# Optimization experiments

Measured on AMD Instinct MI355X. Metric: run time of the kernel, lower is better.

## Reference

```python
import jax, jax.numpy as jnp
import numpy as np

B = 512      # batch
L = 20       # reviews per user/item (L1 == L2)
N = 100      # words per review (must match between user/item, required by original bmm)
V = 50000    # vocab
D = 64       # word_dim
E = 32       # id_emb_size
U = 20000    # user_num
I = 20000    # item_num
H = 3        # point_num_heads
NT, NM = 10, 12  # travel type / month cardinalities


def _lin(x, W, b):
    # torch nn.Linear: x @ W.T + b, W is [out, in]
    return x @ W.T + b


def _hard_gumbel(logits, g):
    # F.gumbel_softmax(hard=True, tau=1, dim=1); g is pre-sampled standard Gumbel noise
    y = jax.nn.softmax(logits + g, axis=1)
    hard = jax.nn.one_hot(jnp.argmax(y, axis=1), logits.shape[1], dtype=y.dtype)
    return hard - jax.lax.stop_gradient(y) + y  # straight-through


def _coatt(u_fea, i_fea, M, Wu, bu, Wi, bi, pooling, gumbel_noise=None):
    # u_fea: [B, L1, d]; i_fea: [B, L2, d]
    u = _lin(u_fea, Wu, bu)
    i = _lin(i_fea, Wi, bi)
    S = jnp.einsum('bld,de,bme->blm', u, M, i)  # [B, L1, L2]
    if pooling == 'max':
        u_score, i_score = S.max(axis=2), S.max(axis=1)
    else:
        u_score, i_score = S.mean(axis=2), S.mean(axis=1)
    if gumbel_noise is not None:
        gu, gi = gumbel_noise
        p_u, p_i = _hard_gumbel(u_score, gu), _hard_gumbel(i_score, gi)
    else:
        p_u, p_i = jax.nn.softmax(u_score, axis=1), jax.nn.softmax(i_score, axis=1)
    return p_u[..., None], p_i[..., None]  # [B, L1, 1], [B, L2, 1]


def setup_inputs() -> dict:
    key = jax.random.key(0)
    ks = iter(jax.random.split(key, 48))
    unif = lambda shape, s=0.1: jax.random.uniform(next(ks), shape, minval=-s, maxval=s, dtype=jnp.float32)
    xav = lambda shape: jax.random.normal(next(ks), shape, dtype=jnp.float32) * np.sqrt(2.0 / (shape[-1] + shape[-2]))
    inp = {}
    inp['user_reviews'] = jax.random.randint(next(ks), (B, L, N), 0, V)
    inp['item_reviews'] = jax.random.randint(next(ks), (B, L, N), 0, V)
    inp['uids'] = jax.random.randint(next(ks), (B,), 0, U)
    inp['iids'] = jax.random.randint(next(ks), (B,), 0, I)
    inp['travel_type'] = jax.random.randint(next(ks), (B,), 0, NT)
    inp['travel_month'] = jax.random.randint(next(ks), (B,), 0, NM)
    # pre-sampled standard Gumbel noise for the hard pointer selection (one per head)
    inp['gnoise_u'] = -jnp.log(-jnp.log(jax.random.uniform(next(ks), (H, B, L), minval=1e-20, maxval=1.0)))
    inp['gnoise_i'] = -jnp.log(-jnp.log(jax.random.uniform(next(ks), (H, B, L), minval=1e-20, maxval=1.0)))
    # embedding tables
    inp['user_word_embs'] = unif((V, D))
    inp['item_word_embs'] = unif((V, D))
    inp['user_id_table'] = unif((U, E), 1.0)
    inp['item_id_table'] = unif((I, E), 1.0)
    inp['type_table'] = unif((NT, E), 1.0)
    inp['month_table'] = unif((NM, E), 1.0)
    # review gate
    inp['fc_g1_w'] = unif((D, D)); inp['fc_g1_b'] = unif((D,))
    inp['fc_g2_w'] = unif((D, D)); inp['fc_g2_b'] = unif((D,))
    # per-head co-attention params (stacked over H)
    inp['M_r'] = xav((H, D, D)); inp['Wu_r'] = unif((H, D, D)); inp['bu_r'] = unif((H, D))
    inp['Wi_r'] = unif((H, D, D)); inp['bi_r'] = unif((H, D))
    inp['M_w'] = xav((H, D, D)); inp['Wu_w'] = unif((H, D, D)); inp['bu_w'] = unif((H, D))
    inp['Wi_w'] = unif((H, D, D)); inp['bi_w'] = unif((H, D))
    inp['M_f'] = xav((H, E, E)); inp['Wu_f'] = unif((H, E, E)); inp['bu_f'] = unif((H, E))
    inp['Wi_f'] = unif((H, E, E)); inp['bi_f'] = unif((H, E))
    # projection layers
    inp['ufc_w'] = unif((E, D)); inp['ufc_b'] = unif((E,))
    inp['ifc_w'] = unif((E, D)); inp['ifc_b'] = unif((E,))
    inp['u_fc_w'] = unif((E, E * H)); inp['u_fc_b'] = unif((E,))
    inp['i_fc_w'] = unif((E, E * H)); inp['i_fc_b'] = unif((E,))
    return inp


def reference(user_reviews, item_reviews, uids, iids, travel_type, travel_month,
              gnoise_u, gnoise_i, user_word_embs, item_word_embs,
              user_id_table, item_id_table, type_table, month_table,
              fc_g1_w, fc_g1_b, fc_g2_w, fc_g2_b,
              M_r, Wu_r, bu_r, Wi_r, bi_r,
              M_w, Wu_w, bu_w, Wi_w, bi_w,
              M_f, Wu_f, bu_f, Wi_f, bi_f,
              ufc_w, ufc_b, ifc_w, ifc_b, u_fc_w, u_fc_b, i_fc_w, i_fc_b):
    # id-type embeddings -> feature stack [B, 4, E]
    user_id_emb = user_id_table[uids]
    item_id_emb = item_id_table[iids]
    type_emb = type_table[travel_type]
    month_emb = month_table[travel_month]
    feature_embedding = jnp.stack([user_id_emb, item_id_emb, type_emb, month_emb], axis=1)

    def review_gate(reviews_idx, table):
        s = table[reviews_idx].sum(axis=2)  # [B, L, N, D] -> [B, L, D]
        return jax.nn.sigmoid(_lin(s, fc_g1_w, fc_g1_b)) * jnp.tanh(_lin(s, fc_g2_w, fc_g2_b))

    u_reviews_g = review_gate(user_reviews, user_word_embs)
    i_reviews_g = review_gate(item_reviews, item_word_embs)

    u_feas, i_feas = [], []
    for h in range(H):
        # review-level pointer co-attention (hard gumbel, max pooling)
        p_u, p_i = _coatt(u_reviews_g, i_reviews_g, M_r[h], Wu_r[h], bu_r[h], Wi_r[h], bi_r[h],
                          pooling='max', gumbel_noise=(gnoise_u[h], gnoise_i[h]))
        # soft index -> cast to int (kills gradient, like torch .long()) -> word gather
        u_idx = jnp.einsum('bln,bl->bn', user_reviews.astype(p_u.dtype), p_u[..., 0]).astype(jnp.int32)
        i_idx = jnp.einsum('bln,bl->bn', item_reviews.astype(p_i.dtype), p_i[..., 0]).astype(jnp.int32)
        u_words = user_word_embs[u_idx]  # [B, N, D]
        i_words = item_word_embs[i_idx]
        # word-level co-attention (softmax, avg pooling)
        p_u2, p_i2 = _coatt(u_words, i_words, M_w[h], Wu_w[h], bu_w[h], Wi_w[h], bi_w[h], pooling='avg')
        u_w_fea = jnp.einsum('bnd,bn->bd', u_words, p_u2[..., 0])
        i_w_fea = jnp.einsum('bnd,bn->bd', u_words, p_i2[..., 0])  # NOTE: original uses u_words here (kept)
        ure = jax.nn.relu(_lin(u_w_fea, ufc_w, ufc_b))  # dropout = identity (eval)
        ire = jax.nn.relu(_lin(i_w_fea, ifc_w, ifc_b))
        review_embedding = jnp.stack([ure, ire], axis=1)  # [B, 2, E]
        review_att, fea_att = _coatt(review_embedding, feature_embedding,
                                     M_f[h], Wu_f[h], bu_f[h], Wi_f[h], bi_f[h], pooling='avg')
        fea_att_e = feature_embedding * fea_att  # [B, 4, E]
        user_id_e, item_id_e, type_e, month_e = (fea_att_e[:, 0], fea_att_e[:, 1],
                                                 fea_att_e[:, 2], fea_att_e[:, 3])
        rae = review_embedding * review_att
        user_fea_h = rae[:, 0]
        u_feas.append(user_fea_h)
        i_feas.append(user_fea_h)  # NOTE: original assigns item_fea from the user slice (kept)
    u_out = _lin(jnp.concatenate(u_feas, axis=1), u_fc_w, u_fc_b)
    i_out = _lin(jnp.concatenate(i_feas, axis=1), i_fc_w, i_fc_b)
    user_fea = jnp.stack([user_id_e, type_e, u_out], axis=1)   # [B, 3, E]
    item_fea = jnp.stack([item_id_e, month_e, i_out], axis=1)  # [B, 3, E]
    return user_fea, item_fea
```

## Files before the change

kernel.cpp:

```cpp
#include <hip/hip_runtime.h>
#include <math.h>

#define Bn 512
#define Ln 20
#define Nn 100
#define Dn 64
#define En 32
#define Hn 3

__global__ __launch_bounds__(256) void k0a_prep(
    const float* __restrict__ M_r, const float* __restrict__ Wu_r, const float* __restrict__ bu_r,
    const float* __restrict__ Wi_r,
    const float* __restrict__ M_w, const float* __restrict__ Wu_w, const float* __restrict__ bu_w,
    const float* __restrict__ Wi_w, const float* __restrict__ bi_w,
    const float* __restrict__ Wu_f, const float* __restrict__ Wi_f,
    const float* __restrict__ ufc, const float* __restrict__ ifc,
    const float* __restrict__ ufc2, const float* __restrict__ ifc2,
    float* __restrict__ WiT_r, float* __restrict__ WMr, float* __restrict__ bMr,
    float* __restrict__ P, float* __restrict__ Q, float* __restrict__ MB, float* __restrict__ MTB,
    float* __restrict__ WuT_f, float* __restrict__ WiT_f,
    float* __restrict__ ufcT, float* __restrict__ ifcT,
    float* __restrict__ u_fcT, float* __restrict__ i_fcT)
{
    int t = blockIdx.x * blockDim.x + threadIdx.x;
    int stride = gridDim.x * blockDim.x;
    for (int k = t; k < Hn*Dn*Dn; k += stride) {
        int h = k >> 12, r = k & 4095; int c = r >> 6, e = r & 63;
        const float* Wu = Wu_r + h*4096; const float* M = M_r + h*4096;
        float a = 0.f;
        for (int d = 0; d < Dn; ++d) a += Wu[d*Dn + c] * M[d*Dn + e];
        WMr[k] = a;
    }
    for (int k = t; k < Hn*Dn*Dn; k += stride) {
        int h = k >> 12, r = k & 4095; int d = r >> 6, bb = r & 63;
        const float* M = M_w + h*4096; const float* Wi = Wi_w + h*4096;
        float a = 0.f;
        for (int e = 0; e < Dn; ++e) a += M[d*Dn + e] * Wi[e*Dn + bb];
        P[k] = a;
    }
    for (int k = t; k < Hn*Dn*Dn; k += stride) {
        int h = k >> 12, r = k & 4095; int d = r >> 6, bb = r & 63;
        const float* M = M_w + h*4096; const float* Wu = Wu_w + h*4096;
        float a = 0.f;
        for (int e = 0; e < Dn; ++e) a += M[e*Dn + d] * Wu[e*Dn + bb];
        Q[k] = a;
    }
    for (int k = t; k < Hn*Dn*Dn; k += stride) {
        int h = k >> 12, r = k & 4095; int c = r >> 6, dp = r & 63;
        WiT_r[k] = Wi_r[h*4096 + dp*Dn + c];
    }
    for (int k = t; k < Hn*Dn; k += stride) {
        int h = k >> 6, e = k & 63;
        const float* M = M_r + h*4096;
        float a = 0.f;
        for (int d = 0; d < Dn; ++d) a += bu_r[h*Dn + d] * M[d*Dn + e];
        bMr[k] = a;
        const float* Mw_ = M_w + h*4096;
        float p = 0.f, q = 0.f;
        for (int d2 = 0; d2 < Dn; ++d2) {
            p += Mw_[e*Dn + d2] * bi_w[h*Dn + d2];
            q += Mw_[d2*Dn + e] * bu_w[h*Dn + d2];
        }
        MB[k] = p; MTB[k] = q;
    }
    for (int k = t; k < Hn*En*En; k += stride) {
        int h = k / (En*En); int rem = k - h*En*En;
        int a = rem >> 5, c = rem & 31;
        int src = h*En*En + c*En + a;
        WuT_f[k] = Wu_f[src]; WiT_f[k] = Wi_f[src];
    }
    for (int k = t; k < Dn*En; k += stride) {
        int d = k >> 5, e = k & 31;
        ufcT[k] = ufc[e*Dn + d]; ifcT[k] = ifc[e*Dn + d];
    }
    for (int k = t; k < 96*En; k += stride) {
        int kk = k >> 5, e = k & 31;
        u_fcT[k] = ufc2[e*96 + kk]; i_fcT[k] = ifc2[e*96 + kk];
    }
}

__global__ __launch_bounds__(256) void k0b_prep(
    const float* __restrict__ Wu_w, const float* __restrict__ Wi_w,
    const float* __restrict__ P, const float* __restrict__ Q,
    const float* __restrict__ MB, const float* __restrict__ MTB,
    float* __restrict__ GuT, float* __restrict__ GiT,
    float* __restrict__ gu_v, float* __restrict__ gi_v)
{
    int t = blockIdx.x * blockDim.x + threadIdx.x;
    int stride = gridDim.x * blockDim.x;
    for (int k = t; k < Hn*Dn*Dn; k += stride) {
        int h = k >> 12, r = k & 4095; int bb = r >> 6, a = r & 63;
        const float* Wu = Wu_w + h*4096; const float* Pp = P + h*4096;
        float s = 0.f;
        for (int d = 0; d < Dn; ++d) s += Wu[d*Dn + a] * Pp[d*Dn + bb];
        GuT[k] = s;
    }
    for (int k = t; k < Hn*Dn*Dn; k += stride) {
        int h = k >> 12, r = k & 4095; int bb = r >> 6, a = r & 63;
        const float* Wi = Wi_w + h*4096; const float* Qp = Q + h*4096;
        float s = 0.f;
        for (int d = 0; d < Dn; ++d) s += Wi[d*Dn + a] * Qp[d*Dn + bb];
        GiT[k] = s;
    }
    for (int k = t; k < Hn*Dn; k += stride) {
        int h = k >> 6, a = k & 63;
        const float* Wu = Wu_w + h*4096; const float* Wi = Wi_w + h*4096;
        float s1 = 0.f, s2 = 0.f;
        for (int d = 0; d < Dn; ++d) {
            s1 += Wu[d*Dn + a] * MB[h*Dn + d];
            s2 += Wi[d*Dn + a] * MTB[h*Dn + d];
        }
        gu_v[k] = s1; gi_v[k] = s2;
    }
}

__global__ __launch_bounds__(256) void k1a_gsum(
    const int* __restrict__ urev, const int* __restrict__ irev,
    const float* __restrict__ utab, const float* __restrict__ itab,
    float* __restrict__ sout)
{
    int tid = threadIdx.x;
    int ln = tid & 63;
    int wv = tid >> 6;
    int gw = blockIdx.x * 4 + wv;
    int side = (gw >= Bn*Ln);
    int r = gw - (side ? Bn*Ln : 0);
    const int* rev = side ? irev : urev;
    const float* tab = side ? itab : utab;
    int i0 = rev[r*Nn + ln];
    int i1 = (ln < Nn - 64) ? rev[r*Nn + 64 + ln] : 0;
    int r0 = ln >> 4;
    int q4 = (ln & 15) << 2;
    float4 buf[25];
    #pragma unroll
    for (int j = 0; j < 25; ++j) {
        int n = r0 + 4*j;
        int idx = (n < 64) ? __shfl(i0, n) : __shfl(i1, n - 64);
        buf[j] = *(const float4*)(tab + idx*Dn + q4);
    }
    float4 a = buf[0];
    #pragma unroll
    for (int j = 1; j < 25; ++j) { a.x += buf[j].x; a.y += buf[j].y; a.z += buf[j].z; a.w += buf[j].w; }
    a.x += __shfl_xor(a.x, 16); a.y += __shfl_xor(a.y, 16); a.z += __shfl_xor(a.z, 16); a.w += __shfl_xor(a.w, 16);
    a.x += __shfl_xor(a.x, 32); a.y += __shfl_xor(a.y, 32); a.z += __shfl_xor(a.z, 32); a.w += __shfl_xor(a.w, 32);
    if (ln < 16) *(float4*)(sout + gw*Dn + q4) = a;
}

__global__ __launch_bounds__(256) void k1b_gate(
    const float* __restrict__ sin,
    const float* __restrict__ W1, const float* __restrict__ b1v,
    const float* __restrict__ W2, const float* __restrict__ b2v,
    float* __restrict__ ugo, float* __restrict__ igo)
{
    __shared__ float w1s[Dn][Dn+1];
    __shared__ float w2s[Dn][Dn+1];
    int tid = threadIdx.x;
    for (int k = tid; k < Dn*Dn; k += 256) {
        int r = k >> 6, c = k & 63;
        w1s[r][c] = W1[k]; w2s[r][c] = W2[k];
    }
    __syncthreads();
    int ln = tid & 63;
    int wv = tid >> 6;
    float b1 = b1v[ln], b2 = b2v[ln];
    int nW = gridDim.x * 4;
    for (int gw = blockIdx.x * 4 + wv; gw < 2*Bn*Ln; gw += nW) {
        float sv = sin[gw*Dn + ln];
        float t1 = b1, t2 = b2;
        #pragma unroll 8
        for (int d = 0; d < Dn; ++d) {
            float sd = __shfl(sv, d);
            t1 += sd * w1s[ln][d];
            t2 += sd * w2s[ln][d];
        }
        float g = (1.f / (1.f + expf(-t1))) * tanhf(t2);
        int side = (gw >= Bn*Ln);
        int r = gw - (side ? Bn*Ln : 0);
        (side ? igo : ugo)[r*Dn + ln] = g;
    }
}

__global__ __launch_bounds__(256, 4) void k2_coatt(
    const int* __restrict__ urev, const int* __restrict__ irev,
    const int* __restrict__ uids, const int* __restrict__ iids,
    const int* __restrict__ ttype, const int* __restrict__ tmonth,
    const float* __restrict__ gu_all, const float* __restrict__ gi_all,
    const float* __restrict__ utab, const float* __restrict__ itab,
    const float* __restrict__ uid_tab, const float* __restrict__ iid_tab,
    const float* __restrict__ type_tab, const float* __restrict__ month_tab,
    const float* __restrict__ ug_in, const float* __restrict__ ig_in,
    const float* __restrict__ WMr, const float* __restrict__ bMr,
    const float* __restrict__ WiT_r, const float* __restrict__ bi_r,
    const float* __restrict__ GuT, const float* __restrict__ GiT,
    const float* __restrict__ gu_v, const float* __restrict__ gi_v,
    const float* __restrict__ M_f, const float* __restrict__ bu_f, const float* __restrict__ bi_f,
    const float* __restrict__ WuT_f, const float* __restrict__ WiT_f,
    const float* __restrict__ ufcT, const float* __restrict__ ufc_bv,
    const float* __restrict__ ifcT, const float* __restrict__ ifc_bv,
    float* __restrict__ feas, float* __restrict__ outp)
{
    __shared__ __align__(16) float pool[6400];
    __shared__ float vecs[4][Dn];
    __shared__ float sc[2][Nn];
    __shared__ float uif[2][Dn];
    __shared__ float att[6];
    __shared__ int   lstar[2];

    int tid = threadIdx.x;
    int bh = blockIdx.x;
    int b = bh / Hn;
    int h = bh - b*Hn;
    int ln = tid & 63;
    int wv = tid >> 6;

    {
        const float4* su = (const float4*)(ug_in + b*Ln*Dn);
        const float4* si = (const float4*)(ig_in + b*Ln*Dn);
        float4* du = (float4*)pool;
        float4* di = (float4*)(pool + 1280);
        for (int k = tid; k < (Ln*Dn)/4; k += 256) { du[k] = su[k]; di[k] = si[k]; }
    }
    __syncthreads();

    {
        int iside = wv >> 1;
        int lbase = (wv & 1) * 10;
        const float* W = (iside ? (WiT_r + h*4096) : (WMr + h*4096)) + ln;
        const float* X = pool + (iside ? 1280 : 0);
        float bias = iside ? bi_r[h*Dn + ln] : bMr[h*Dn + ln];
        float acc[10];
        #pragma unroll
        for (int l = 0; l < 10; ++l) acc[l] = 0.f;
        for (int dd = 0; dd < Dn; dd += 4) {
            float w0 = W[(dd+0)*Dn];
            float w1 = W[(dd+1)*Dn];
            float w2 = W[(dd+2)*Dn];
            float w3 = W[(dd+3)*Dn];
            #pragma unroll
            for (int l = 0; l < 10; ++l) {
                float4 x = *(const float4*)(X + (lbase+l)*Dn + dd);
                acc[l] += x.x*w0 + x.y*w1 + x.z*w2 + x.w*w3;
            }
        }
        float* out = pool + (iside ? 3840 : 2560);
        #pragma unroll
        for (int l = 0; l < 10; ++l) {
            int lg = lbase + l;
            out[lg*Dn + (ln ^ lg)] = acc[l] + bias;
        }
    }
    __syncthreads();
    for (int k = tid; k < Ln*Ln; k += 256) {
        int l = k / Ln, m = k - l*Ln;
        const float* Ab = pool + 2560 + l*Dn;
        const float* iv = pool + 3840 + m*Dn;
        float a = 0.f;
        for (int e = 0; e < Dn; ++e) a += Ab[e ^ l] * iv[e ^ m];
        pool[5120 + k] = a;
    }
    __syncthreads();
    if (wv == 0) {
        float v = -3.4e38f;
        if (ln < Ln) {
            float mx = pool[5120 + ln*Ln];
            #pragma unroll
            for (int m = 1; m < Ln; ++m) mx = fmaxf(mx, pool[5120 + ln*Ln + m]);
            v = mx + gu_all[(h*Bn + b)*Ln + ln];
        }
        int idx = ln;
        #pragma unroll
        for (int off = 32; off > 0; off >>= 1) {
            float ov = __shfl_down(v, off);
            int oi = __shfl_down(idx, off);
            if (ov > v || (ov == v && oi < idx)) { v = ov; idx = oi; }
        }
        if (ln == 0) lstar[0] = idx;
    } else if (wv == 1) {
        float v = -3.4e38f;
        if (ln < Ln) {
            float mx = pool[5120 + ln];
            #pragma unroll
            for (int l = 1; l < Ln; ++l) mx = fmaxf(mx, pool[5120 + l*Ln + ln]);
            v = mx + gi_all[(h*Bn + b)*Ln + ln];
        }
        int idx = ln;
        #pragma unroll
        for (int off = 32; off > 0; off >>= 1) {
            float ov = __shfl_down(v, off);
            int oi = __shfl_down(idx, off);
            if (ov > v || (ov == v && oi < idx)) { v = ov; idx = oi; }
        }
        if (ln == 0) lstar[1] = idx;
    }
    __syncthreads();

    int rubase = (b*Ln + lstar[0])*Nn;
    int ribase = (b*Ln + lstar[1])*Nn;
    int r0 = ln >> 4;
    int q4 = (ln & 15) << 2;
    int idxr[25];

    if (wv < 2) {
        for (int k = tid; k < Nn*16; k += 128) {
            int n = k >> 4, qi = k & 15;
            int idx = urev[rubase + n];
            float4 v = *(const float4*)(utab + idx*Dn + (qi << 2));
            *(float4*)(pool + n*Dn + (((qi ^ (n & 15)) << 2))) = v;
        }
    } else {
        const int* rev = (wv == 2) ? irev : urev;
        const float* tab = (wv == 2) ? itab : utab;
        int rb = (wv == 2) ? ribase : rubase;
        #pragma unroll
        for (int j = 0; j < 25; ++j) idxr[j] = rev[rb + r0 + 4*j];
        float4 s = make_float4(0.f, 0.f, 0.f, 0.f);
        #pragma unroll 5
        for (int g = 0; g < 5; ++g) {
            float4 v0 = *(const float4*)(tab + idxr[g*5+0]*Dn + q4);
            float4 v1 = *(const float4*)(tab + idxr[g*5+1]*Dn + q4);
            float4 v2 = *(const float4*)(tab + idxr[g*5+2]*Dn + q4);
            float4 v3 = *(const float4*)(tab + idxr[g*5+3]*Dn + q4);
            float4 v4 = *(const float4*)(tab + idxr[g*5+4]*Dn + q4);
            s.x += v0.x+v1.x+v2.x+v3.x+v4.x;
            s.y += v0.y+v1.y+v2.y+v3.y+v4.y;
            s.z += v0.z+v1.z+v2.z+v3.z+v4.z;
            s.w += v0.w+v1.w+v2.w+v3.w+v4.w;
        }
        s.x += __shfl_xor(s.x, 16); s.y += __shfl_xor(s.y, 16); s.z += __shfl_xor(s.z, 16); s.w += __shfl_xor(s.w, 16);
        s.x += __shfl_xor(s.x, 32); s.y += __shfl_xor(s.y, 32); s.z += __shfl_xor(s.z, 32); s.w += __shfl_xor(s.w, 32);
        if (ln < 16) {
            float4 m = make_float4(s.x*(1.f/Nn), s.y*(1.f/Nn), s.z*(1.f/Nn), s.w*(1.f/Nn));
            *(float4*)(&vecs[(wv == 2) ? 1 : 0][q4]) = m;
        }
    }
    __syncthreads();

    if (tid < Dn) {
        float a = gu_v[h*Dn + tid];
        for (int bb = 0; bb < Dn; ++bb) a += GuT[h*4096 + bb*Dn + tid] * vecs[1][bb];
        vecs[2][tid] = a;
    } else if (tid < 2*Dn) {
        int aa = tid - Dn;
        float a = gi_v[h*Dn + aa];
        for (int bb = 0; bb < Dn; ++bb) a += GiT[h*4096 + bb*Dn + aa] * vecs[0][bb];
        vecs[3][aa] = a;
    }
    __syncthreads();

    if (tid < Nn) {
        float a = 0.f;
        const float* row = pool + tid*Dn;
        int sw = tid & 15;
        #pragma unroll
        for (int qi = 0; qi < 16; ++qi) {
            float4 w = *(const float4*)(&vecs[2][qi << 2]);
            float4 x = *(const float4*)(row + ((qi ^ sw) << 2));
            a += x.x*w.x + x.y*w.y + x.z*w.z + x.w*w.w;
        }
        sc[0][tid] = a;
    } else if (wv == 2) {
        float4 wq = *(const float4*)(&vecs[3][q4]);
        #pragma unroll 5
        for (int g = 0; g < 5; ++g) {
            float p0, p1, p2, p3, p4;
            {
                float4 v0 = *(const float4*)(itab + idxr[g*5+0]*Dn + q4);
                float4 v1 = *(const float4*)(itab + idxr[g*5+1]*Dn + q4);
                float4 v2 = *(const float4*)(itab + idxr[g*5+2]*Dn + q4);
                float4 v3 = *(const float4*)(itab + idxr[g*5+3]*Dn + q4);
                float4 v4 = *(const float4*)(itab + idxr[g*5+4]*Dn + q4);
                p0 = v0.x*wq.x + v0.y*wq.y + v0.z*wq.z + v0.w*wq.w;
                p1 = v1.x*wq.x + v1.y*wq.y + v1.z*wq.z + v1.w*wq.w;
                p2 = v2.x*wq.x + v2.y*wq.y + v2.z*wq.z + v2.w*wq.w;
                p3 = v3.x*wq.x + v3.y*wq.y + v3.z*wq.z + v3.w*wq.w;
                p4 = v4.x*wq.x + v4.y*wq.y + v4.z*wq.z + v4.w*wq.w;
            }
            #pragma unroll
            for (int off = 1; off < 16; off <<= 1) {
                p0 += __shfl_xor(p0, off); p1 += __shfl_xor(p1, off);
                p2 += __shfl_xor(p2, off); p3 += __shfl_xor(p3, off);
                p4 += __shfl_xor(p4, off);
            }
            if ((ln & 15) == 0) {
                sc[1][r0 + 4*(g*5+0)] = p0;
                sc[1][r0 + 4*(g*5+1)] = p1;
                sc[1][r0 + 4*(g*5+2)] = p2;
                sc[1][r0 + 4*(g*5+3)] = p3;
                sc[1][r0 + 4*(g*5+4)] = p4;
            }
        }
    }
    __syncthreads();
    if (wv == 0 || wv == 2) {
        float* s = sc[wv >> 1];
        float x0 = s[ln];
        float x1 = (ln < Nn - 64) ? s[64 + ln] : -3.4e38f;
        float mx = fmaxf(x0, x1);
        #pragma unroll
        for (int off = 32; off > 0; off >>= 1) mx = fmaxf(mx, __shfl_xor(mx, off));
        float e0 = expf(x0 - mx);
        float e1 = (ln < Nn - 64) ? expf(x1 - mx) : 0.f;
        float sum = e0 + e1;
        #pragma unroll
        for (int off = 32; off > 0; off >>= 1) sum += __shfl_xor(sum, off);
        float inv = 1.f / sum;
        s[ln] = e0 * inv;
        if (ln < Nn - 64) s[64 + ln] = e1 * inv;
    }
    __syncthreads();
    if (tid < 2*Dn) {
        int which = tid >> 6;
        int d = tid & 63;
        int qt = (d >> 2), dl = d & 3;
        const float* p = sc[which];
        float a = 0.f;
        for (int n = 0; n < Nn; ++n)
            a += p[n] * pool[n*Dn + ((qt ^ (n & 15)) << 2) + dl];
        uif[which][d] = a;
    }
    __syncthreads();
    float* fe_ = pool;
    float* re_ = pool + 128;
    float* u3_ = pool + 192;
    float* i3_ = pool + 256;
    float* A3_ = pool + 384;
    if (tid < En) {
        float a = ufc_bv[tid];
        for (int d = 0; d < Dn; ++d) a += uif[0][d] * ufcT[d*En + tid];
        re_[tid] = fmaxf(a, 0.f);
    } else if (tid < 2*En) {
        int e = tid - En;
        float a = ifc_bv[e];
        for (int d = 0; d < Dn; ++d) a += uif[1][d] * ifcT[d*En + e];
        re_[En + e] = fmaxf(a, 0.f);
    } else if (tid < 2*En + 4*En) {
        int j = tid - 2*En;
        int rrow = j >> 5, e = j & 31;
        float v;
        if (rrow == 0) v = uid_tab[uids[b]*En + e];
        else if (rrow == 1) v = iid_tab[iids[b]*En + e];
        else if (rrow == 2) v = type_tab[ttype[b]*En + e];
        else v = month_tab[tmonth[b]*En + e];
        fe_[j] = v;
    }
    __syncthreads();
    const float* WuTf = WuT_f + h*En*En;
    const float* WiTf = WiT_f + h*En*En;
    const float* Mf   = M_f  + h*En*En;
    if (tid < 2*En) {
        int l = tid >> 5, e = tid & 31;
        float a = bu_f[h*En + e];
        for (int j = 0; j < En; ++j) a += re_[l*En + j] * WuTf[j*En + e];
        u3_[tid] = a;
    } else if (tid < 6*En) {
        int t2 = tid - 2*En;
        int m = t2 >> 5, e = t2 & 31;
        float a = bi_f[h*En + e];
        for (int j = 0; j < En; ++j) a += fe_[m*En + j] * WiTf[j*En + e];
        i3_[t2] = a;
    }
    __syncthreads();
    if (tid < 2*En) {
        int l = tid >> 5, e = tid & 31;
        float a = 0.f;
        for (int d = 0; d < En; ++d) a += u3_[l*En + d] * Mf[d*En + e];
        A3_[tid] = a;
    }
    __syncthreads();
    if (tid == 0) {
        float S3[2][4];
        for (int l = 0; l < 2; ++l)
            for (int m = 0; m < 4; ++m) {
                float a = 0.f;
                for (int e = 0; e < En; ++e) a += A3_[l*En + e] * i3_[m*En + e];
                S3[l][m] = a;
            }
        float us0 = (S3[0][0] + S3[0][1] + S3[0][2] + S3[0][3]) * 0.25f;
        float us1 = (S3[1][0] + S3[1][1] + S3[1][2] + S3[1][3]) * 0.25f;
        float mx = fmaxf(us0, us1);
        float e0 = expf(us0 - mx), e1 = expf(us1 - mx);
        float inv = 1.f / (e0 + e1);
        att[0] = e0 * inv; att[1] = e1 * inv;
        float is_[4]; float mxi = -3.4e38f;
        for (int m = 0; m < 4; ++m) { is_[m] = (S3[0][m] + S3[1][m]) * 0.5f; mxi = fmaxf(mxi, is_[m]); }
        float ssum = 0.f, ee[4];
        for (int m = 0; m < 4; ++m) { ee[m] = expf(is_[m] - mxi); ssum += ee[m]; }
        float invi = 1.f / ssum;
        for (int m = 0; m < 4; ++m) att[2 + m] = ee[m] * invi;
    }
    __syncthreads();
    if (tid < En) {
        feas[b*96 + h*En + tid] = re_[tid] * att[0];
    }
    if (h == 2) {
        if (tid >= 32 && tid < 64)        { int e = tid - 32;  outp[b*96 + e]              = fe_[e]      * att[2]; }
        else if (tid >= 64 && tid < 96)   { int e = tid - 64;  outp[b*96 + 32 + e]         = fe_[64 + e] * att[4]; }
        else if (tid >= 96 && tid < 128)  { int e = tid - 96;  outp[Bn*96 + b*96 + e]      = fe_[32 + e] * att[3]; }
        else if (tid >= 128 && tid < 160) { int e = tid - 128; outp[Bn*96 + b*96 + 32 + e] = fe_[96 + e] * att[5]; }
    }
}

__global__ __launch_bounds__(64) void k3_final(
    const float* __restrict__ feas,
    const float* __restrict__ u_fcT, const float* __restrict__ u_fc_bv,
    const float* __restrict__ i_fcT, const float* __restrict__ i_fc_bv,
    float* __restrict__ outp)
{
    __shared__ float f[96];
    int b = blockIdx.x, tid = threadIdx.x;
    for (int k = tid; k < 96; k += 64) f[k] = feas[b*96 + k];
    __syncthreads();
    if (tid < 32) {
        float a = u_fc_bv[tid];
        for (int k = 0; k < 96; ++k) a += f[k] * u_fcT[k*32 + tid];
        outp[b*96 + 64 + tid] = a;
    } else {
        int e = tid - 32;
        float a = i_fc_bv[e];
        for (int k = 0; k < 96; ++k) a += f[k] * i_fcT[k*32 + e];
        outp[Bn*96 + b*96 + 64 + e] = a;
    }
}

extern "C" void kernel_launch(void* const* d_in, const int* in_sizes, int n_in,
                              void* d_out, int out_size, void* d_ws, size_t ws_size,
                              hipStream_t stream)
{
    const int* urev = (const int*)d_in[0];
    const int* irev = (const int*)d_in[1];
    const int* uids = (const int*)d_in[2];
    const int* iids = (const int*)d_in[3];
    const int* ttype = (const int*)d_in[4];
    const int* tmonth = (const int*)d_in[5];
    const float* gu = (const float*)d_in[6];
    const float* gi = (const float*)d_in[7];
    const float* utab = (const float*)d_in[8];
    const float* itab = (const float*)d_in[9];
    const float* uid_tab = (const float*)d_in[10];
    const float* iid_tab = (const float*)d_in[11];
    const float* type_tab = (const float*)d_in[12];
    const float* month_tab = (const float*)d_in[13];
    const float* fc_g1_w = (const float*)d_in[14];
    const float* fc_g1_b = (const float*)d_in[15];
    const float* fc_g2_w = (const float*)d_in[16];
    const float* fc_g2_b = (const float*)d_in[17];
    const float* M_r = (const float*)d_in[18];
    const float* Wu_r = (const float*)d_in[19];
    const float* bu_r = (const float*)d_in[20];
    const float* Wi_r = (const float*)d_in[21];
    const float* bi_r = (const float*)d_in[22];
    const float* M_w = (const float*)d_in[23];
    const float* Wu_w = (const float*)d_in[24];
    const float* bu_w = (const float*)d_in[25];
    const float* Wi_w = (const float*)d_in[26];
    const float* bi_w = (const float*)d_in[27];
    const float* M_f = (const float*)d_in[28];
    const float* Wu_f = (const float*)d_in[29];
    const float* bu_f = (const float*)d_in[30];
    const float* Wi_f = (const float*)d_in[31];
    const float* bi_f = (const float*)d_in[32];
    const float* ufc_w = (const float*)d_in[33];
    const float* ufc_b = (const float*)d_in[34];
    const float* ifc_w = (const float*)d_in[35];
    const float* ifc_b = (const float*)d_in[36];
    const float* u_fc_w = (const float*)d_in[37];
    const float* u_fc_b = (const float*)d_in[38];
    const float* i_fc_w = (const float*)d_in[39];
    const float* i_fc_b = (const float*)d_in[40];
    (void)in_sizes; (void)n_in; (void)out_size; (void)ws_size;

    float* ws = (float*)d_ws;
    float* ugo   = ws;
    float* igo   = ugo + Bn*Ln*Dn;
    float* sgat  = igo + Bn*Ln*Dn;
    float* feas  = sgat + 2*Bn*Ln*Dn;
    float* WiT_r = feas + Bn*96;
    float* WMr   = WiT_r + Hn*Dn*Dn;
    float* bMr   = WMr + Hn*Dn*Dn;
    float* P     = bMr + Hn*Dn;
    float* Q     = P + Hn*Dn*Dn;
    float* MB    = Q + Hn*Dn*Dn;
    float* MTB   = MB + Hn*Dn;
    float* GuT   = MTB + Hn*Dn;
    float* GiT   = GuT + Hn*Dn*Dn;
    float* gu_v  = GiT + Hn*Dn*Dn;
    float* gi_v  = gu_v + Hn*Dn;
    float* WuT_f = gi_v + Hn*Dn;
    float* WiT_f = WuT_f + Hn*En*En;
    float* ufcT  = WiT_f + Hn*En*En;
    float* ifcT  = ufcT + Dn*En;
    float* u_fcT = ifcT + Dn*En;
    float* i_fcT = u_fcT + 96*En;

    hipLaunchKernelGGL(k0a_prep, dim3(48), dim3(256), 0, stream,
        M_r, Wu_r, bu_r, Wi_r, M_w, Wu_w, bu_w, Wi_w, bi_w,
        Wu_f, Wi_f, ufc_w, ifc_w, u_fc_w, i_fc_w,
        WiT_r, WMr, bMr, P, Q, MB, MTB, WuT_f, WiT_f, ufcT, ifcT, u_fcT, i_fcT);

    hipLaunchKernelGGL(k0b_prep, dim3(48), dim3(256), 0, stream,
        Wu_w, Wi_w, P, Q, MB, MTB, GuT, GiT, gu_v, gi_v);

    hipLaunchKernelGGL(k1a_gsum, dim3(2*Bn*Ln/4), dim3(256), 0, stream,
        urev, irev, utab, itab, sgat);

    hipLaunchKernelGGL(k1b_gate, dim3(512), dim3(256), 0, stream,
        sgat, fc_g1_w, fc_g1_b, fc_g2_w, fc_g2_b, ugo, igo);

    hipLaunchKernelGGL(k2_coatt, dim3(Bn*Hn), dim3(256), 0, stream,
        urev, irev, uids, iids, ttype, tmonth, gu, gi, utab, itab,
        uid_tab, iid_tab, type_tab, month_tab, ugo, igo,
        WMr, bMr, WiT_r, bi_r, GuT, GiT, gu_v, gi_v,
        M_f, bu_f, bi_f, WuT_f, WiT_f,
        ufcT, ufc_b, ifcT, ifc_b, feas, (float*)d_out);

    hipLaunchKernelGGL(k3_final, dim3(Bn), dim3(64), 0, stream,
        feas, u_fcT, u_fc_b, i_fcT, i_fc_b, (float*)d_out);
}
```

Baseline: 326.7 us.

## Fuse weight-folding prep kernels into one LDS-staged per-head kernel

Replaces the two grid-stride prep kernels (P/Q, then GuT/GiT) with a single kernel that stages each head's M, Wu and Wi matrices in shared memory and computes the intermediate products there, splitting outputs across 4 blocks per head. This removes the global round trip for P, Q, MB and MTB and one kernel launch. Each of the 4 blocks per head redundantly computes the full P/Q intermediates, and only 12 blocks run, so the work is less spread across the device. Transposes move into a separate small kernel.

New measurement: 347.5 us. +6.4%, slower.

```diff
diff --git a/kernel.cpp b/kernel.cpp
--- a/kernel.cpp
+++ b/kernel.cpp
@@ -8,16 +8,97 @@
 #define En 32
 #define Hn 3
 
-__global__ __launch_bounds__(256) void k0a_prep(
+__global__ __launch_bounds__(256) void k0_fold(
     const float* __restrict__ M_r, const float* __restrict__ Wu_r, const float* __restrict__ bu_r,
-    const float* __restrict__ Wi_r,
     const float* __restrict__ M_w, const float* __restrict__ Wu_w, const float* __restrict__ bu_w,
     const float* __restrict__ Wi_w, const float* __restrict__ bi_w,
+    float* __restrict__ WMr, float* __restrict__ bMr,
+    float* __restrict__ GuT, float* __restrict__ GiT,
+    float* __restrict__ gu_v, float* __restrict__ gi_v)
+{
+    __shared__ float A[4096], B2[4096], C2[4096], D2[4096], E2[4096];
+    __shared__ float MBs[64], MTBs[64];
+    int tid = threadIdx.x;
+    int h = blockIdx.x >> 2, sub = blockIdx.x & 3;
+    {
+        const float4* a = (const float4*)(M_w + h*4096);
+        const float4* bsrc = (const float4*)(Wu_w + h*4096);
+        const float4* c = (const float4*)(Wi_w + h*4096);
+        for (int k = tid; k < 1024; k += 256) {
+            ((float4*)A)[k] = a[k];
+            ((float4*)B2)[k] = bsrc[k];
+            ((float4*)C2)[k] = c[k];
+        }
+    }
+    __syncthreads();
+    for (int k = tid; k < 4096; k += 256) {
+        int d = k >> 6, b = k & 63;
+        float p = 0.f, q = 0.f;
+        for (int e = 0; e < 64; ++e) {
+            p += A[d*64 + e] * C2[e*64 + b];
+            q += A[e*64 + d] * B2[e*64 + b];
+        }
+        D2[k] = p; E2[k] = q;
+    }
+    if (sub == 0 && tid < 64) {
+        float p = 0.f, q = 0.f;
+        for (int e = 0; e < 64; ++e) {
+            p += A[tid*64 + e] * bi_w[h*64 + e];
+            q += A[e*64 + tid] * bu_w[h*64 + e];
+        }
+        MBs[tid] = p; MTBs[tid] = q;
+    }
+    __syncthreads();
+    #pragma unroll
+    for (int i = 0; i < 4; ++i) {
+        int k = sub*1024 + i*256 + tid;
+        int b = k >> 6, a = k & 63;
+        float s1 = 0.f, s2 = 0.f;
+        for (int d = 0; d < 64; ++d) {
+            s1 += B2[d*64 + a] * D2[d*64 + b];
+            s2 += C2[d*64 + a] * E2[d*64 + b];
+        }
+        GuT[h*4096 + k] = s1; GiT[h*4096 + k] = s2;
+    }
+    if (sub == 0 && tid < 64) {
+        float s1 = 0.f, s2 = 0.f;
+        for (int d = 0; d < 64; ++d) {
+            s1 += B2[d*64 + tid] * MBs[d];
+            s2 += C2[d*64 + tid] * MTBs[d];
+        }
+        gu_v[h*64 + tid] = s1; gi_v[h*64 + tid] = s2;
+    }
+    __syncthreads();
+    {
+        const float4* a = (const float4*)(M_r + h*4096);
+        const float4* bsrc = (const float4*)(Wu_r + h*4096);
+        for (int k = tid; k < 1024; k += 256) {
+            ((float4*)A)[k] = a[k];
+            ((float4*)B2)[k] = bsrc[k];
+        }
+    }
+    __syncthreads();
+    #pragma unroll
+    for (int i = 0; i < 4; ++i) {
+        int k = sub*1024 + i*256 + tid;
+        int c = k >> 6, e = k & 63;
+        float s = 0.f;
+        for (int d = 0; d < 64; ++d) s += B2[d*64 + c] * A[d*64 + e];
+        WMr[h*4096 + k] = s;
+    }
+    if (sub == 0 && tid < 64) {
+        float s = 0.f;
+        for (int d = 0; d < 64; ++d) s += bu_r[h*64 + d] * A[d*64 + tid];
+        bMr[h*64 + tid] = s;
+    }
+}
+
+__global__ __launch_bounds__(256) void k0_misc(
+    const float* __restrict__ Wi_r,
     const float* __restrict__ Wu_f, const float* __restrict__ Wi_f,
     const float* __restrict__ ufc, const float* __restrict__ ifc,
     const float* __restrict__ ufc2, const float* __restrict__ ifc2,
-    float* __restrict__ WiT_r, float* __restrict__ WMr, float* __restrict__ bMr,
-    float* __restrict__ P, float* __restrict__ Q, float* __restrict__ MB, float* __restrict__ MTB,
+    float* __restrict__ WiT_r,
     float* __restrict__ WuT_f, float* __restrict__ WiT_f,
     float* __restrict__ ufcT, float* __restrict__ ifcT,
     float* __restrict__ u_fcT, float* __restrict__ i_fcT)
@@ -25,43 +106,8 @@
     int t = blockIdx.x * blockDim.x + threadIdx.x;
     int stride = gridDim.x * blockDim.x;
     for (int k = t; k < Hn*Dn*Dn; k += stride) {
-        int h = k >> 12, r = k & 4095; int c = r >> 6, e = r & 63;
-        const float* Wu = Wu_r + h*4096; const float* M = M_r + h*4096;
-        float a = 0.f;
-        for (int d = 0; d < Dn; ++d) a += Wu[d*Dn + c] * M[d*Dn + e];
-        WMr[k] = a;
-    }
-    for (int k = t; k < Hn*Dn*Dn; k += stride) {
-        int h = k >> 12, r = k & 4095; int d = r >> 6, bb = r & 63;
-        const float* M = M_w + h*4096; const float* Wi = Wi_w + h*4096;
-        float a = 0.f;
-        for (int e = 0; e < Dn; ++e) a += M[d*Dn + e] * Wi[e*Dn + bb];
-        P[k] = a;
-    }
-    for (int k = t; k < Hn*Dn*Dn; k += stride) {
-        int h = k >> 12, r = k & 4095; int d = r >> 6, bb = r & 63;
-        const float* M = M_w + h*4096; const float* Wu = Wu_w + h*4096;
-        float a = 0.f;
-        for (int e = 0; e < Dn; ++e) a += M[e*Dn + d] * Wu[e*Dn + bb];
-        Q[k] = a;
-    }
-    for (int k = t; k < Hn*Dn*Dn; k += stride) {
         int h = k >> 12, r = k & 4095; int c = r >> 6, dp = r & 63;
         WiT_r[k] = Wi_r[h*4096 + dp*Dn + c];
-    }
-    for (int k = t; k < Hn*Dn; k += stride) {
-        int h = k >> 6, e = k & 63;
-        const float* M = M_r + h*4096;
-        float a = 0.f;
-        for (int d = 0; d < Dn; ++d) a += bu_r[h*Dn + d] * M[d*Dn + e];
-        bMr[k] = a;
-        const float* Mw_ = M_w + h*4096;
-        float p = 0.f, q = 0.f;
-        for (int d2 = 0; d2 < Dn; ++d2) {
-            p += Mw_[e*Dn + d2] * bi_w[h*Dn + d2];
-            q += Mw_[d2*Dn + e] * bu_w[h*Dn + d2];
-        }
-        MB[k] = p; MTB[k] = q;
     }
     for (int k = t; k < Hn*En*En; k += stride) {
         int h = k / (En*En); int rem = k - h*En*En;
@@ -76,41 +122,6 @@
     for (int k = t; k < 96*En; k += stride) {
         int kk = k >> 5, e = k & 31;
         u_fcT[k] = ufc2[e*96 + kk]; i_fcT[k] = ifc2[e*96 + kk];
-    }
-}
-
-__global__ __launch_bounds__(256) void k0b_prep(
-    const float* __restrict__ Wu_w, const float* __restrict__ Wi_w,
-    const float* __restrict__ P, const float* __restrict__ Q,
-    const float* __restrict__ MB, const float* __restrict__ MTB,
-    float* __restrict__ GuT, float* __restrict__ GiT,
-    float* __restrict__ gu_v, float* __restrict__ gi_v)
-{
-    int t = blockIdx.x * blockDim.x + threadIdx.x;
-    int stride = gridDim.x * blockDim.x;
-    for (int k = t; k < Hn*Dn*Dn; k += stride) {
-        int h = k >> 12, r = k & 4095; int bb = r >> 6, a = r & 63;
-        const float* Wu = Wu_w + h*4096; const float* Pp = P + h*4096;
-        float s = 0.f;
-        for (int d = 0; d < Dn; ++d) s += Wu[d*Dn + a] * Pp[d*Dn + bb];
-        GuT[k] = s;
-    }
-    for (int k = t; k < Hn*Dn*Dn; k += stride) {
-        int h = k >> 12, r = k & 4095; int bb = r >> 6, a = r & 63;
-        const float* Wi = Wi_w + h*4096; const float* Qp = Q + h*4096;
-        float s = 0.f;
-        for (int d = 0; d < Dn; ++d) s += Wi[d*Dn + a] * Qp[d*Dn + bb];
-        GiT[k] = s;
-    }
-    for (int k = t; k < Hn*Dn; k += stride) {
-        int h = k >> 6, a = k & 63;
-        const float* Wu = Wu_w + h*4096; const float* Wi = Wi_w + h*4096;
-        float s1 = 0.f, s2 = 0.f;
-        for (int d = 0; d < Dn; ++d) {
-            s1 += Wu[d*Dn + a] * MB[h*Dn + d];
-            s2 += Wi[d*Dn + a] * MTB[h*Dn + d];
-        }
-        gu_v[k] = s1; gi_v[k] = s2;
     }
 }
 
@@ -577,11 +588,7 @@
     float* WiT_r = feas + Bn*96;
     float* WMr   = WiT_r + Hn*Dn*Dn;
     float* bMr   = WMr + Hn*Dn*Dn;
-    float* P     = bMr + Hn*Dn;
-    float* Q     = P + Hn*Dn*Dn;
-    float* MB    = Q + Hn*Dn*Dn;
-    float* MTB   = MB + Hn*Dn;
-    float* GuT   = MTB + Hn*Dn;
+    float* GuT   = bMr + Hn*Dn;
     float* GiT   = GuT + Hn*Dn*Dn;
     float* gu_v  = GiT + Hn*Dn*Dn;
     float* gi_v  = gu_v + Hn*Dn;
@@ -592,13 +599,13 @@
     float* u_fcT = ifcT + Dn*En;
     float* i_fcT = u_fcT + 96*En;
 
-    hipLaunchKernelGGL(k0a_prep, dim3(48), dim3(256), 0, stream,
-        M_r, Wu_r, bu_r, Wi_r, M_w, Wu_w, bu_w, Wi_w, bi_w,
-        Wu_f, Wi_f, ufc_w, ifc_w, u_fc_w, i_fc_w,
-        WiT_r, WMr, bMr, P, Q, MB, MTB, WuT_f, WiT_f, ufcT, ifcT, u_fcT, i_fcT);
-
-    hipLaunchKernelGGL(k0b_prep, dim3(48), dim3(256), 0, stream,
-        Wu_w, Wi_w, P, Q, MB, MTB, GuT, GiT, gu_v, gi_v);
+    hipLaunchKernelGGL(k0_fold, dim3(Hn*4), dim3(256), 0, stream,
+        M_r, Wu_r, bu_r, M_w, Wu_w, bu_w, Wi_w, bi_w,
+        WMr, bMr, GuT, GiT, gu_v, gi_v);
+
+    hipLaunchKernelGGL(k0_misc, dim3(16), dim3(256), 0, stream,
+        Wi_r, Wu_f, Wi_f, ufc_w, ifc_w, u_fc_w, i_fc_w,
+        WiT_r, WuT_f, WiT_f, ufcT, ifcT, u_fcT, i_fcT);
 
     hipLaunchKernelGGL(k1a_gsum, dim3(2*Bn*Ln/4), dim3(256), 0, stream,
         urev, irev, utab, itab, sgat);
```

## Fuse weight-prep kernels and merge review gather-sum with gating kernel

Applied to the files above, without the earlier changes.

Collapses the two weight-precompute kernels into one block-partitioned kernel. Each wavefront now computes an intermediate row into shared memory and immediately applies the second matmul, so the P/Q/MB/MTB workspace buffers are no longer needed. The embedding gather-sum kernel is merged into the gate kernel, with the summed row passed through a small shared buffer instead of a global workspace. This drops two launches and a 2*B*L*D global round trip, at the cost of a larger per-wave loop over four rows in the gate kernel. There is no barrier between the shared-memory row write and its read within a wave, which relies on wavefront lockstep.

New measurement: 292.6 us. 1.12x faster.

```diff
diff --git a/kernel.cpp b/kernel.cpp
--- a/kernel.cpp
+++ b/kernel.cpp
@@ -8,7 +8,7 @@
 #define En 32
 #define Hn 3
 
-__global__ __launch_bounds__(256) void k0a_prep(
+__global__ __launch_bounds__(256) void k0_all(
     const float* __restrict__ M_r, const float* __restrict__ Wu_r, const float* __restrict__ bu_r,
     const float* __restrict__ Wi_r,
     const float* __restrict__ M_w, const float* __restrict__ Wu_w, const float* __restrict__ bu_w,
@@ -16,166 +16,132 @@
     const float* __restrict__ Wu_f, const float* __restrict__ Wi_f,
     const float* __restrict__ ufc, const float* __restrict__ ifc,
     const float* __restrict__ ufc2, const float* __restrict__ ifc2,
-    float* __restrict__ WiT_r, float* __restrict__ WMr, float* __restrict__ bMr,
-    float* __restrict__ P, float* __restrict__ Q, float* __restrict__ MB, float* __restrict__ MTB,
+    float* __restrict__ WMr, float* __restrict__ bMr,
+    float* __restrict__ GuT, float* __restrict__ GiT,
+    float* __restrict__ gu_v, float* __restrict__ gi_v,
+    float* __restrict__ WiT_r,
     float* __restrict__ WuT_f, float* __restrict__ WiT_f,
     float* __restrict__ ufcT, float* __restrict__ ifcT,
     float* __restrict__ u_fcT, float* __restrict__ i_fcT)
 {
-    int t = blockIdx.x * blockDim.x + threadIdx.x;
-    int stride = gridDim.x * blockDim.x;
-    for (int k = t; k < Hn*Dn*Dn; k += stride) {
-        int h = k >> 12, r = k & 4095; int c = r >> 6, e = r & 63;
-        const float* Wu = Wu_r + h*4096; const float* M = M_r + h*4096;
-        float a = 0.f;
-        for (int d = 0; d < Dn; ++d) a += Wu[d*Dn + c] * M[d*Dn + e];
-        WMr[k] = a;
-    }
-    for (int k = t; k < Hn*Dn*Dn; k += stride) {
-        int h = k >> 12, r = k & 4095; int d = r >> 6, bb = r & 63;
-        const float* M = M_w + h*4096; const float* Wi = Wi_w + h*4096;
-        float a = 0.f;
-        for (int e = 0; e < Dn; ++e) a += M[d*Dn + e] * Wi[e*Dn + bb];
-        P[k] = a;
-    }
-    for (int k = t; k < Hn*Dn*Dn; k += stride) {
-        int h = k >> 12, r = k & 4095; int d = r >> 6, bb = r & 63;
-        const float* M = M_w + h*4096; const float* Wu = Wu_w + h*4096;
-        float a = 0.f;
-        for (int e = 0; e < Dn; ++e) a += M[e*Dn + d] * Wu[e*Dn + bb];
-        Q[k] = a;
-    }
-    for (int k = t; k < Hn*Dn*Dn; k += stride) {
-        int h = k >> 12, r = k & 4095; int c = r >> 6, dp = r & 63;
-        WiT_r[k] = Wi_r[h*4096 + dp*Dn + c];
-    }
-    for (int k = t; k < Hn*Dn; k += stride) {
-        int h = k >> 6, e = k & 63;
-        const float* M = M_r + h*4096;
-        float a = 0.f;
-        for (int d = 0; d < Dn; ++d) a += bu_r[h*Dn + d] * M[d*Dn + e];
-        bMr[k] = a;
-        const float* Mw_ = M_w + h*4096;
-        float p = 0.f, q = 0.f;
-        for (int d2 = 0; d2 < Dn; ++d2) {
-            p += Mw_[e*Dn + d2] * bi_w[h*Dn + d2];
-            q += Mw_[d2*Dn + e] * bu_w[h*Dn + d2];
-        }
-        MB[k] = p; MTB[k] = q;
-    }
-    for (int k = t; k < Hn*En*En; k += stride) {
-        int h = k / (En*En); int rem = k - h*En*En;
-        int a = rem >> 5, c = rem & 31;
-        int src = h*En*En + c*En + a;
-        WuT_f[k] = Wu_f[src]; WiT_f[k] = Wi_f[src];
-    }
-    for (int k = t; k < Dn*En; k += stride) {
-        int d = k >> 5, e = k & 31;
-        ufcT[k] = ufc[e*Dn + d]; ifcT[k] = ifc[e*Dn + d];
-    }
-    for (int k = t; k < 96*En; k += stride) {
-        int kk = k >> 5, e = k & 31;
-        u_fcT[k] = ufc2[e*96 + kk]; i_fcT[k] = ifc2[e*96 + kk];
+    __shared__ float tbuf[4][64];
+    int tid = threadIdx.x, ln = tid & 63, wv = tid >> 6;
+    int blk = blockIdx.x;
+    if (blk < 48) {
+        int W = blk*4 + wv;
+        int h = W >> 6, c = W & 63;
+        const float* Wu = Wu_r + h*4096;
+        const float* M  = M_r  + h*4096;
+        float s = 0.f;
+        for (int d = 0; d < 64; ++d) s += Wu[d*64 + c] * M[d*64 + ln];
+        WMr[h*4096 + c*64 + ln] = s;
+    } else if (blk < 51) {
+        int h = blk - 48;
+        if (wv == 0) {
+            float s = 0.f;
+            for (int d = 0; d < 64; ++d) s += bu_r[h*64 + d] * M_r[h*4096 + d*64 + ln];
+            bMr[h*64 + ln] = s;
+        }
+    } else if (blk < 147) {
+        int W = (blk - 51)*4 + wv;
+        int isGi = (W >= 192);
+        int W2 = W - (isGi ? 192 : 0);
+        int h = W2 >> 6, a = W2 & 63;
+        float t;
+        if (!isGi) {
+            const float* Wu = Wu_w + h*4096; const float* M = M_w + h*4096;
+            t = 0.f;
+            for (int d = 0; d < 64; ++d) t += Wu[d*64 + a] * M[d*64 + ln];
+        } else {
+            const float* Wi = Wi_w + h*4096; const float* M = M_w + h*4096;
+            t = 0.f;
+            for (int d = 0; d < 64; ++d) t += M[ln*64 + d] * Wi[d*64 + a];
+        }
+        tbuf[wv][ln] = t;
+        const float* Wsec = (isGi ? Wu_w : Wi_w) + h*4096;
+        const float* bsec = (isGi ? bu_w : bi_w) + h*64;
+        float s = 0.f, gvv = 0.f;
+        for (int e = 0; e < 64; ++e) {
+            float te = tbuf[wv][e];
+            s   += te * Wsec[e*64 + ln];
+            gvv += te * bsec[e];
+        }
+        (isGi ? GiT : GuT)[h*4096 + ln*64 + a] = s;
+        if (ln == 0) (isGi ? gi_v : gu_v)[h*64 + a] = gvv;
+    } else if (blk < 195) {
+        int k = (blk - 147)*256 + tid;
+        int h = k >> 12, r = k & 4095, c = r >> 6, dp = r & 63;
+        WiT_r[k] = Wi_r[h*4096 + dp*64 + c];
+    } else {
+        int t = (blk - 195)*256 + tid;
+        int stride = 8*256;
+        for (int k = t; k < Hn*En*En; k += stride) {
+            int h = k/(En*En); int rem = k - h*En*En;
+            int aa = rem >> 5, c = rem & 31;
+            int src = h*En*En + c*En + aa;
+            WuT_f[k] = Wu_f[src]; WiT_f[k] = Wi_f[src];
+        }
+        for (int k = t; k < Dn*En; k += stride) {
+            int d = k >> 5, e = k & 31;
+            ufcT[k] = ufc[e*Dn + d]; ifcT[k] = ifc[e*Dn + d];
+        }
+        for (int k = t; k < 96*En; k += stride) {
+            int kk = k >> 5, e = k & 31;
+            u_fcT[k] = ufc2[e*96 + kk]; i_fcT[k] = ifc2[e*96 + kk];
+        }
     }
 }
 
-__global__ __launch_bounds__(256) void k0b_prep(
-    const float* __restrict__ Wu_w, const float* __restrict__ Wi_w,
-    const float* __restrict__ P, const float* __restrict__ Q,
-    const float* __restrict__ MB, const float* __restrict__ MTB,
-    float* __restrict__ GuT, float* __restrict__ GiT,
-    float* __restrict__ gu_v, float* __restrict__ gi_v)
-{
-    int t = blockIdx.x * blockDim.x + threadIdx.x;
-    int stride = gridDim.x * blockDim.x;
-    for (int k = t; k < Hn*Dn*Dn; k += stride) {
-        int h = k >> 12, r = k & 4095; int bb = r >> 6, a = r & 63;
-        const float* Wu = Wu_w + h*4096; const float* Pp = P + h*4096;
-        float s = 0.f;
-        for (int d = 0; d < Dn; ++d) s += Wu[d*Dn + a] * Pp[d*Dn + bb];
-        GuT[k] = s;
-    }
-    for (int k = t; k < Hn*Dn*Dn; k += stride) {
-        int h = k >> 12, r = k & 4095; int bb = r >> 6, a = r & 63;
-        const float* Wi = Wi_w + h*4096; const float* Qp = Q + h*4096;
-        float s = 0.f;
-        for (int d = 0; d < Dn; ++d) s += Wi[d*Dn + a] * Qp[d*Dn + bb];
-        GiT[k] = s;
-    }
-    for (int k = t; k < Hn*Dn; k += stride) {
-        int h = k >> 6, a = k & 63;
-        const float* Wu = Wu_w + h*4096; const float* Wi = Wi_w + h*4096;
-        float s1 = 0.f, s2 = 0.f;
-        for (int d = 0; d < Dn; ++d) {
-            s1 += Wu[d*Dn + a] * MB[h*Dn + d];
-            s2 += Wi[d*Dn + a] * MTB[h*Dn + d];
-        }
-        gu_v[k] = s1; gi_v[k] = s2;
-    }
-}
-
-__global__ __launch_bounds__(256) void k1a_gsum(
+__global__ __launch_bounds__(256) void k1_gate2(
     const int* __restrict__ urev, const int* __restrict__ irev,
     const float* __restrict__ utab, const float* __restrict__ itab,
-    float* __restrict__ sout)
-{
-    int tid = threadIdx.x;
-    int ln = tid & 63;
-    int wv = tid >> 6;
-    int gw = blockIdx.x * 4 + wv;
-    int side = (gw >= Bn*Ln);
-    int r = gw - (side ? Bn*Ln : 0);
-    const int* rev = side ? irev : urev;
-    const float* tab = side ? itab : utab;
-    int i0 = rev[r*Nn + ln];
-    int i1 = (ln < Nn - 64) ? rev[r*Nn + 64 + ln] : 0;
-    int r0 = ln >> 4;
-    int q4 = (ln & 15) << 2;
-    float4 buf[25];
-    #pragma unroll
-    for (int j = 0; j < 25; ++j) {
-        int n = r0 + 4*j;
-        int idx = (n < 64) ? __shfl(i0, n) : __shfl(i1, n - 64);
-        buf[j] = *(const float4*)(tab + idx*Dn + q4);
-    }
-    float4 a = buf[0];
-    #pragma unroll
-    for (int j = 1; j < 25; ++j) { a.x += buf[j].x; a.y += buf[j].y; a.z += buf[j].z; a.w += buf[j].w; }
-    a.x += __shfl_xor(a.x, 16); a.y += __shfl_xor(a.y, 16); a.z += __shfl_xor(a.z, 16); a.w += __shfl_xor(a.w, 16);
-    a.x += __shfl_xor(a.x, 32); a.y += __shfl_xor(a.y, 32); a.z += __shfl_xor(a.z, 32); a.w += __shfl_xor(a.w, 32);
-    if (ln < 16) *(float4*)(sout + gw*Dn + q4) = a;
-}
-
-__global__ __launch_bounds__(256) void k1b_gate(
-    const float* __restrict__ sin,
     const float* __restrict__ W1, const float* __restrict__ b1v,
     const float* __restrict__ W2, const float* __restrict__ b2v,
     float* __restrict__ ugo, float* __restrict__ igo)
 {
     __shared__ float w1s[Dn][Dn+1];
     __shared__ float w2s[Dn][Dn+1];
+    __shared__ float rowb[4][Dn];
     int tid = threadIdx.x;
     for (int k = tid; k < Dn*Dn; k += 256) {
-        int r = k >> 6, c = k & 63;
-        w1s[r][c] = W1[k]; w2s[r][c] = W2[k];
-    }
-    __syncthreads();
-    int ln = tid & 63;
-    int wv = tid >> 6;
+        w1s[k>>6][k&63] = W1[k];
+        w2s[k>>6][k&63] = W2[k];
+    }
+    __syncthreads();
+    int ln = tid & 63, wv = tid >> 6;
+    int wid = blockIdx.x * 4 + wv;
+    int r0 = ln >> 4, q4 = (ln & 15) << 2;
     float b1 = b1v[ln], b2 = b2v[ln];
-    int nW = gridDim.x * 4;
-    for (int gw = blockIdx.x * 4 + wv; gw < 2*Bn*Ln; gw += nW) {
-        float sv = sin[gw*Dn + ln];
+    #pragma unroll 1
+    for (int it = 0; it < 4; ++it) {
+        int gw = wid + it * 5120;
+        int side = (gw >= Bn*Ln);
+        int r = gw - (side ? Bn*Ln : 0);
+        const int* rev = side ? irev : urev;
+        const float* tab = side ? itab : utab;
+        int i0 = rev[r*Nn + ln];
+        int i1 = (ln < Nn - 64) ? rev[r*Nn + 64 + ln] : 0;
+        float4 buf[25];
+        #pragma unroll
+        for (int j = 0; j < 25; ++j) {
+            int n = r0 + 4*j;
+            int idx = (n < 64) ? __shfl(i0, n) : __shfl(i1, n - 64);
+            buf[j] = *(const float4*)(tab + idx*Dn + q4);
+        }
+        float4 a = buf[0];
+        #pragma unroll
+        for (int j = 1; j < 25; ++j) { a.x += buf[j].x; a.y += buf[j].y; a.z += buf[j].z; a.w += buf[j].w; }
+        a.x += __shfl_xor(a.x, 16); a.y += __shfl_xor(a.y, 16); a.z += __shfl_xor(a.z, 16); a.w += __shfl_xor(a.w, 16);
+        a.x += __shfl_xor(a.x, 32); a.y += __shfl_xor(a.y, 32); a.z += __shfl_xor(a.z, 32); a.w += __shfl_xor(a.w, 32);
+        if (ln < 16) *(float4*)(&rowb[wv][q4]) = a;
         float t1 = b1, t2 = b2;
         #pragma unroll 8
         for (int d = 0; d < Dn; ++d) {
-            float sd = __shfl(sv, d);
+            float sd = rowb[wv][d];
             t1 += sd * w1s[ln][d];
             t2 += sd * w2s[ln][d];
         }
         float g = (1.f / (1.f + expf(-t1))) * tanhf(t2);
-        int side = (gw >= Bn*Ln);
-        int r = gw - (side ? Bn*Ln : 0);
         (side ? igo : ugo)[r*Dn + ln] = g;
     }
 }
@@ -572,16 +538,11 @@
     float* ws = (float*)d_ws;
     float* ugo   = ws;
     float* igo   = ugo + Bn*Ln*Dn;
-    float* sgat  = igo + Bn*Ln*Dn;
-    float* feas  = sgat + 2*Bn*Ln*Dn;
+    float* feas  = igo + Bn*Ln*Dn;
     float* WiT_r = feas + Bn*96;
     float* WMr   = WiT_r + Hn*Dn*Dn;
     float* bMr   = WMr + Hn*Dn*Dn;
-    float* P     = bMr + Hn*Dn;
-    float* Q     = P + Hn*Dn*Dn;
-    float* MB    = Q + Hn*Dn*Dn;
-    float* MTB   = MB + Hn*Dn;
-    float* GuT   = MTB + Hn*Dn;
+    float* GuT   = bMr + Hn*Dn;
     float* GiT   = GuT + Hn*Dn*Dn;
     float* gu_v  = GiT + Hn*Dn*Dn;
     float* gi_v  = gu_v + Hn*Dn;
@@ -592,19 +553,14 @@
     float* u_fcT = ifcT + Dn*En;
     float* i_fcT = u_fcT + 96*En;
 
-    hipLaunchKernelGGL(k0a_prep, dim3(48), dim3(256), 0, stream,
+    hipLaunchKernelGGL(k0_all, dim3(203), dim3(256), 0, stream,
         M_r, Wu_r, bu_r, Wi_r, M_w, Wu_w, bu_w, Wi_w, bi_w,
         Wu_f, Wi_f, ufc_w, ifc_w, u_fc_w, i_fc_w,
-        WiT_r, WMr, bMr, P, Q, MB, MTB, WuT_f, WiT_f, ufcT, ifcT, u_fcT, i_fcT);
-
-    hipLaunchKernelGGL(k0b_prep, dim3(48), dim3(256), 0, stream,
-        Wu_w, Wi_w, P, Q, MB, MTB, GuT, GiT, gu_v, gi_v);
-
-    hipLaunchKernelGGL(k1a_gsum, dim3(2*Bn*Ln/4), dim3(256), 0, stream,
-        urev, irev, utab, itab, sgat);
-
-    hipLaunchKernelGGL(k1b_gate, dim3(512), dim3(256), 0, stream,
-        sgat, fc_g1_w, fc_g1_b, fc_g2_w, fc_g2_b, ugo, igo);
+        WMr, bMr, GuT, GiT, gu_v, gi_v, WiT_r,
+        WuT_f, WiT_f, ufcT, ifcT, u_fcT, i_fcT);
+
+    hipLaunchKernelGGL(k1_gate2, dim3(1280), dim3(256), 0, stream,
+        urev, irev, utab, itab, fc_g1_w, fc_g1_b, fc_g2_w, fc_g2_b, ugo, igo);
 
     hipLaunchKernelGGL(k2_coatt, dim3(Bn*Hn), dim3(256), 0, stream,
         urev, irev, uids, iids, ttype, tmonth, gu, gi, utab, itab,
```
